# Performance work log

Measured on AMD Instinct MI355X. Metric: run time of the kernel, lower is better.

## Reference

```python
import jax, jax.numpy as jnp
import numpy as np

N = 100_000
E = 1_600_000
IN_DIM = 21
HID = 256
OUT = 256


def setup_inputs() -> dict:
    key = jax.random.key(0)
    ks = jax.random.split(key, 10)
    node_scalar = jax.random.normal(ks[0], (N, IN_DIM), dtype=jnp.float32)
    edge_index = jax.random.randint(ks[1], (2, E), 0, N, dtype=jnp.int64)
    s_in = 1.0 / np.sqrt(IN_DIM)
    s_h = 1.0 / np.sqrt(HID)
    W_in = jax.random.uniform(ks[2], (IN_DIM, HID), jnp.float32, -s_in, s_in)
    b_in = jax.random.uniform(ks[3], (HID,), jnp.float32, -s_in, s_in)
    W_self = jax.random.uniform(ks[4], (HID, HID), jnp.float32, -s_h, s_h)
    b_self = jax.random.uniform(ks[5], (HID,), jnp.float32, -s_h, s_h)
    W_nei = jax.random.uniform(ks[6], (HID, HID), jnp.float32, -s_h, s_h)
    b_nei = jax.random.uniform(ks[7], (HID,), jnp.float32, -s_h, s_h)
    W_out = jax.random.uniform(ks[8], (HID, OUT), jnp.float32, -s_h, s_h)
    b_out = jax.random.uniform(ks[9], (OUT,), jnp.float32, -s_h, s_h)
    return {
        "node_scalar": node_scalar,
        "W_in": W_in, "b_in": b_in,
        "W_self": W_self, "b_self": b_self,
        "W_nei": W_nei, "b_nei": b_nei,
        "W_out": W_out, "b_out": b_out,
        "edge_index": edge_index,
    }


def reference(node_scalar, W_in, b_in, W_self, b_self, W_nei, b_nei, W_out, b_out, edge_index):
    # x = relu(Linear(node_scalar)); dropout is identity in eval mode
    x = jax.nn.relu(node_scalar @ W_in + b_in)           # (N, H)
    n = x.shape[0]
    src, dst = edge_index[0], edge_index[1]
    msg = x[src]                                          # (E, H) gather
    agg = jax.ops.segment_sum(msg, dst, num_segments=n)   # (N, H) scatter-add
    deg = jax.ops.segment_sum(jnp.ones((dst.shape[0],), dtype=x.dtype), dst, num_segments=n)
    agg = agg / jnp.maximum(deg, 1.0)[:, None]            # degree mean (clamp_min 1)
    h = jax.nn.relu(x @ W_self + b_self + agg @ W_nei + b_nei)
    g = h.mean(axis=0)                                    # global mean pool -> (H,)
    return g @ W_out + b_out                              # (OUT,)
```

## Files before the change

kernel.cpp:

```cpp
#include <hip/hip_runtime.h>
#include <hip/hip_bf16.h>

#define HID 256
#define IND 21
#define PB 6400
#define MAXB 512

typedef short short8 __attribute__((ext_vector_type(8)));
typedef float floatx16 __attribute__((ext_vector_type(16)));
typedef float floatx2 __attribute__((ext_vector_type(2)));

__device__ inline unsigned short f2bf(float f) {
  __hip_bfloat16 h = __float2bfloat16(f);
  union { __hip_bfloat16 h; unsigned short u; } c;
  c.h = h;
  return c.u;
}

__device__ inline unsigned int pk_bf16_trunc(floatx2 p) {
  union { float f; unsigned int u; } a, b;
  a.f = p.x; b.f = p.y;
  return (b.u & 0xffff0000u) | (a.u >> 16);
}

__device__ inline void acc8p(uint2 v, floatx2* a) {
  a[0] += __builtin_amdgcn_cvt_pk_f32_fp8((int)v.x, false);
  a[1] += __builtin_amdgcn_cvt_pk_f32_fp8((int)v.x, true);
  a[2] += __builtin_amdgcn_cvt_pk_f32_fp8((int)v.y, false);
  a[3] += __builtin_amdgcn_cvt_pk_f32_fp8((int)v.y, true);
}

__device__ inline short8 mk_s8(unsigned a, unsigned b, unsigned c, unsigned d) {
  union { uint4 u; short8 s; } x; x.u = make_uint4(a, b, c, d); return x.s;
}

__device__ inline short8 dec8(uint2 v) {
  unsigned w0 = pk_bf16_trunc(__builtin_amdgcn_cvt_pk_f32_fp8((int)v.x, false));
  unsigned w1 = pk_bf16_trunc(__builtin_amdgcn_cvt_pk_f32_fp8((int)v.x, true));
  unsigned w2 = pk_bf16_trunc(__builtin_amdgcn_cvt_pk_f32_fp8((int)v.y, false));
  unsigned w3 = pk_bf16_trunc(__builtin_amdgcn_cvt_pk_f32_fp8((int)v.y, true));
  return mk_s8(w0, w1, w2, w3);
}

__device__ inline void gl16(const unsigned char* g, unsigned char* l) {
  __builtin_amdgcn_global_load_lds(
      (const __attribute__((address_space(1))) unsigned char*)g,
      (__attribute__((address_space(3))) unsigned char*)l, 16, 0, 0);
}

__global__ __launch_bounds__(256) void k_front(
    const float* __restrict__ ns, const float* __restrict__ Win,
    const float* __restrict__ bin, unsigned int* __restrict__ xq,
    uint2* __restrict__ Aqx,
    const float* __restrict__ Wself, const float* __restrict__ Wnei,
    unsigned short* __restrict__ Bf16,
    const int* __restrict__ dst, int* __restrict__ bcnt,
    int N, int E, int nb2, int G1) {
  int blk = blockIdx.x;
  int tid = threadIdx.x;
  if (blk < G1) {
    __shared__ float s[8][IND];
    __shared__ float fx[8][257];
    int nb = blk * 8;
    if (tid < 8 * IND) {
      int idx = nb * IND + tid;
      s[tid / IND][tid % IND] = (idx < N * IND) ? ns[idx] : 0.f;
    }
    float w[IND];
#pragma unroll
    for (int k = 0; k < IND; k++) w[k] = Win[k * HID + tid];
    float b = bin[tid];
    __syncthreads();
#pragma unroll
    for (int j = 0; j < 8; j++) {
      float acc = b;
#pragma unroll
      for (int k = 0; k < IND; k++) acc += s[j][k] * w[k];
      fx[j][tid] = acc > 0.f ? acc : 0.f;
    }
    __syncthreads();
#pragma unroll
    for (int t = 0; t < 2; t++) {
      int wi = tid + t * 256;
      int j = wi >> 6, cw = wi & 63;
      int node = nb + j;
      if (node < N) {
        const float* fp = &fx[j][cw * 4];
        int lo = __builtin_amdgcn_cvt_pk_fp8_f32(fp[0], fp[1], 0, false);
        int full = __builtin_amdgcn_cvt_pk_fp8_f32(fp[2], fp[3], lo, true);
        xq[(size_t)node * 64 + cw] = (unsigned int)full;
      }
    }
    {
      int j = tid >> 5, u = tid & 31;
      int node = nb + j;
      if (node < N) {
        const float* fp = &fx[j][u * 8];
        int lo0 = __builtin_amdgcn_cvt_pk_fp8_f32(fp[0], fp[1], 0, false);
        int w0  = __builtin_amdgcn_cvt_pk_fp8_f32(fp[2], fp[3], lo0, true);
        int lo1 = __builtin_amdgcn_cvt_pk_fp8_f32(fp[4], fp[5], 0, false);
        int w1  = __builtin_amdgcn_cvt_pk_fp8_f32(fp[6], fp[7], lo1, true);
        int g = node >> 5, row = node & 31, c = u >> 1, hi = u & 1;
        Aqx[(size_t)(g * 16 + c) * 64 + hi * 32 + row] =
            make_uint2((unsigned)w0, (unsigned)w1);
      }
    }
  } else if (blk < G1 + 256) {
    int n = blk - G1;
    int ct = n >> 5, l5 = n & 31;
#pragma unroll
    for (int t = 0; t < 2; t++) {
      int k = tid + t * 256;
      float v = (k < HID) ? Wself[k * HID + n] : Wnei[(k - HID) * HID + n];
      int c = k >> 4, kin = k & 15;
      int lane = (kin >> 3) * 32 + l5;
      int j = kin & 7;
      Bf16[(size_t)((c * 8 + ct) * 64 + lane) * 8 + j] = f2bf(v);
    }
  } else {
    __shared__ int lh[MAXB];
    int e0 = (blk - G1 - 256) * PB;
    for (int b = tid; b < nb2; b += 256) lh[b] = 0;
    __syncthreads();
    int c = min(PB, E - e0);
    for (int i = tid; i < c; i += 256) atomicAdd(&lh[dst[e0 + i] >> 8], 1);
    __syncthreads();
    for (int b = tid; b < nb2; b += 256)
      if (lh[b]) atomicAdd(&bcnt[b], lh[b]);
  }
}

__global__ __launch_bounds__(512) void k_bscan(
    const int* __restrict__ bcnt, int* __restrict__ bbase, int* __restrict__ bcur,
    int* __restrict__ row_start, int E, int N, int nb2) {
  __shared__ int ts[512];
  int tid = threadIdx.x;
  int v = (tid < nb2) ? bcnt[tid] : 0;
  ts[tid] = v;
  __syncthreads();
  for (int off = 1; off < 512; off <<= 1) {
    int t = (tid >= off) ? ts[tid - off] : 0;
    __syncthreads();
    ts[tid] += t;
    __syncthreads();
  }
  if (tid < nb2) { bbase[tid] = ts[tid] - v; bcur[tid] = ts[tid] - v; }
  if (tid == 0) { bbase[nb2] = E; row_start[N] = E; }
}

__global__ __launch_bounds__(256) void k_part(
    const int* __restrict__ src, const int* __restrict__ dst,
    int* __restrict__ bcur, unsigned int* __restrict__ ebuf, int E, int nb2) {
  __shared__ int lh[MAXB];
  int tid = threadIdx.x;
  int e0 = blockIdx.x * PB;
  for (int b = tid; b < nb2; b += 256) lh[b] = 0;
  __syncthreads();
  int cnt = min(PB, E - e0);
  for (int i = tid; i < cnt; i += 256) atomicAdd(&lh[dst[e0 + i] >> 8], 1);
  __syncthreads();
  for (int b = tid; b < nb2; b += 256) {
    int c = lh[b];
    lh[b] = (c > 0) ? atomicAdd(&bcur[b], c) : 0;
  }
  __syncthreads();
  for (int i = tid; i < cnt; i += 256) {
    int s = src[e0 + i];
    int d = dst[e0 + i];
    int pos = atomicAdd(&lh[d >> 8], 1);
    ebuf[pos] = ((unsigned)s << 8) | ((unsigned)d & 255u);
  }
}

__global__ __launch_bounds__(256) void k_fill2(
    const unsigned int* __restrict__ ebuf, const int* __restrict__ bbase,
    int* __restrict__ row_start, int* __restrict__ csr, int N) {
  __shared__ int lcnt[256];
  __shared__ int lcur[256];
  __shared__ int ts[256];
  int b = blockIdx.x;
  int tid = threadIdx.x;
  int start = bbase[b], end = bbase[b + 1];
  lcnt[tid] = 0;
  __syncthreads();
  for (int i = start + tid; i < end; i += 256)
    atomicAdd(&lcnt[ebuf[i] & 255u], 1);
  __syncthreads();
  int v = lcnt[tid];
  ts[tid] = v;
  __syncthreads();
  for (int off = 1; off < 256; off <<= 1) {
    int t = (tid >= off) ? ts[tid - off] : 0;
    __syncthreads();
    ts[tid] += t;
    __syncthreads();
  }
  int excl = start + ts[tid] - v;
  int node = (b << 8) + tid;
  if (node < N) row_start[node] = excl;
  lcur[tid] = excl;
  __syncthreads();
  for (int i = start + tid; i < end; i += 256) {
    unsigned int e = ebuf[i];
    int pos = atomicAdd(&lcur[e & 255u], 1);
    csr[pos] = (int)(e >> 8);
  }
}

__global__ __launch_bounds__(256) void k_agg(
    const uint2* __restrict__ xq, const int* __restrict__ csr,
    const int* __restrict__ row_start, uint2* __restrict__ aggq, int N) {
  int wid = (int)((blockIdx.x * (unsigned)blockDim.x + threadIdx.x) >> 6);
  int lane = threadIdx.x & 63;
  int half = lane >> 5;
  int l32 = lane & 31;
  if (wid >= N) return;
  int start = row_start[wid];
  int end = row_start[wid + 1];
  int c = end - start;
  floatx2 a[4], b[4], d[4], e[4];
#pragma unroll
  for (int j = 0; j < 4; j++) {
    a[j] = (floatx2){0.f, 0.f}; b[j] = (floatx2){0.f, 0.f};
    d[j] = (floatx2){0.f, 0.f}; e[j] = (floatx2){0.f, 0.f};
  }
  int i = 0;
  for (; i + 8 <= c; i += 8) {
    int s0 = csr[start + i + half];
    int s1 = csr[start + i + 2 + half];
    int s2 = csr[start + i + 4 + half];
    int s3 = csr[start + i + 6 + half];
    uint2 v0 = xq[(size_t)s0 * 32 + l32];
    uint2 v1 = xq[(size_t)s1 * 32 + l32];
    uint2 v2 = xq[(size_t)s2 * 32 + l32];
    uint2 v3 = xq[(size_t)s3 * 32 + l32];
    acc8p(v0, a); acc8p(v1, b); acc8p(v2, d); acc8p(v3, e);
  }
  for (; i + 2 <= c; i += 2) {
    int s0 = csr[start + i + half];
    uint2 v0 = xq[(size_t)s0 * 32 + l32];
    acc8p(v0, a);
  }
  if ((c & 1) && half == 0) {
    int s0 = csr[start + c - 1];
    uint2 v0 = xq[(size_t)s0 * 32 + l32];
    acc8p(v0, a);
  }
#pragma unroll
  for (int j = 0; j < 4; j++) a[j] += b[j] + d[j] + e[j];

  float f[8];
#pragma unroll
  for (int j = 0; j < 4; j++) { f[2 * j] = a[j].x; f[2 * j + 1] = a[j].y; }
#pragma unroll
  for (int j = 0; j < 8; j++) f[j] += __shfl_xor(f[j], 32);

  if (half == 0) {
    float inv = 1.0f / fmaxf((float)c, 1.0f);
#pragma unroll
    for (int j = 0; j < 8; j++) f[j] *= inv;
    int lo0 = __builtin_amdgcn_cvt_pk_fp8_f32(f[0], f[1], 0, false);
    int w0  = __builtin_amdgcn_cvt_pk_fp8_f32(f[2], f[3], lo0, true);
    int lo1 = __builtin_amdgcn_cvt_pk_fp8_f32(f[4], f[5], 0, false);
    int w1  = __builtin_amdgcn_cvt_pk_fp8_f32(f[6], f[7], lo1, true);
    int g = wid >> 5, row = wid & 31, cc = l32 >> 1, hi = l32 & 1;
    aggq[(size_t)(g * 16 + cc) * 64 + hi * 32 + row] =
        make_uint2((unsigned)w0, (unsigned)w1);
  }
}

__global__ __launch_bounds__(256, 3) void k_h(
    const unsigned char* __restrict__ Aqx, const unsigned char* __restrict__ Aqagg,
    const unsigned char* __restrict__ Bf8, const float* __restrict__ bself,
    const float* __restrict__ bnei, float* __restrict__ gsum, int N) {
  __shared__ __align__(16) unsigned char As[2][8192];
  __shared__ __align__(16) unsigned char Bs[2][16384];
  __shared__ float colsum[128];
  int tid = threadIdx.x;
  int lane = tid & 63;
  int w = tid >> 6;
  int wr = w >> 1, wc = w & 1;
  int l32 = lane & 31, half = lane >> 5;
  int bx = blockIdx.x, by = blockIdx.y;
  int rowBase = bx * 128;

  if (tid < 128) colsum[tid] = 0.f;

  floatx16 acc[2][2];
#pragma unroll
  for (int i = 0; i < 2; i++)
#pragma unroll
    for (int j = 0; j < 2; j++) acc[i][j] = (floatx16)(0.f);

  size_t a_grp = (size_t)(bx * 4 + w) * 16 * 512;
  int lb = lane * 16;

  {
    const unsigned char* asrc = Aqx + a_grp + lb;
    gl16(asrc, As[0] + w * 2048);
    gl16(asrc + 1024, As[0] + w * 2048 + 1024);
#pragma unroll
    for (int fi = 0; fi < 4; fi++) {
      int cg = w;
      int ctg = by * 4 + fi;
      gl16(Bf8 + (size_t)(cg * 8 + ctg) * 1024 + lb, Bs[0] + (w * 4 + fi) * 1024);
    }
  }

  for (int ch = 0; ch < 8; ch++) {
    int buf = ch & 1;
    __syncthreads();
    if (ch < 7) {
      int cn = ch + 1;
      const unsigned char* Aq = (cn < 4) ? Aqx : Aqagg;
      const unsigned char* asrc = Aq + a_grp + (size_t)(cn & 3) * 2048 + lb;
      unsigned char* ad = As[buf ^ 1] + w * 2048;
      gl16(asrc, ad);
      gl16(asrc + 1024, ad + 1024);
#pragma unroll
      for (int fi = 0; fi < 4; fi++) {
        int cg = cn * 4 + w;
        int ctg = by * 4 + fi;
        gl16(Bf8 + (size_t)(cg * 8 + ctg) * 1024 + lb,
             Bs[buf ^ 1] + (w * 4 + fi) * 1024);
      }
    }
#pragma unroll
    for (int cl = 0; cl < 4; cl++) {
      short8 afr[2];
#pragma unroll
      for (int rt = 0; rt < 2; rt++) {
        uint2 av = *(const uint2*)&As[buf][(wr * 2 + rt) * 2048 + cl * 512 + lane * 8];
        afr[rt] = dec8(av);
      }
#pragma unroll
      for (int ctw = 0; ctw < 2; ctw++) {
        short8 bfr = *(const short8*)&Bs[buf][(cl * 4 + wc * 2 + ctw) * 1024 + lane * 16];
#pragma unroll
        for (int rt = 0; rt < 2; rt++)
          acc[rt][ctw] = __builtin_amdgcn_mfma_f32_32x32x16_bf16(
              afr[rt], bfr, acc[rt][ctw], 0, 0, 0);
      }
    }
  }

#pragma unroll
  for (int ctw = 0; ctw < 2; ctw++) {
    int lcol = (wc * 2 + ctw) * 32 + l32;
    int gcol = by * 128 + lcol;
    float bb = bself[gcol] + bnei[gcol];
    float psum = 0.f;
#pragma unroll
    for (int rt = 0; rt < 2; rt++) {
#pragma unroll
      for (int r = 0; r < 16; r++) {
        int rw = rowBase + wr * 64 + rt * 32 + (r & 3) + 8 * (r >> 2) + 4 * half;
        float v = acc[rt][ctw][r] + bb;
        v = v > 0.f ? v : 0.f;
        if (rw < N) psum += v;
      }
    }
    atomicAdd(&colsum[lcol], psum);
  }
  __syncthreads();
  if (tid < 128) atomicAdd(&gsum[by * 128 + tid], colsum[tid]);
}

__global__ __launch_bounds__(HID) void k_out(
    const float* __restrict__ gsum, const float* __restrict__ Wout,
    const float* __restrict__ bout, float* __restrict__ out, float invN) {
  __shared__ float g[HID];
  int c = threadIdx.x;
  g[c] = gsum[c] * invN;
  __syncthreads();
  float acc = bout[c];
#pragma unroll 8
  for (int k = 0; k < HID; k++) acc += g[k] * Wout[k * HID + c];
  out[c] = acc;
}

extern "C" void kernel_launch(void* const* d_in, const int* in_sizes, int n_in,
                              void* d_out, int out_size, void* d_ws, size_t ws_size,
                              hipStream_t stream) {
  const float* ns    = (const float*)d_in[0];
  const float* Win   = (const float*)d_in[1];
  const float* bin   = (const float*)d_in[2];
  const float* Wself = (const float*)d_in[3];
  const float* bself = (const float*)d_in[4];
  const float* Wnei  = (const float*)d_in[5];
  const float* bnei  = (const float*)d_in[6];
  const float* Wout  = (const float*)d_in[7];
  const float* bout  = (const float*)d_in[8];
  const int*   eidx  = (const int*)d_in[9];

  int N = in_sizes[0] / IND;
  int E = in_sizes[9] / 2;
  const int* src = eidx;
  const int* dst = eidx + E;
  int nb2 = (N + 255) >> 8;
  int nbx = (N + 127) / 128;
  size_t NGU = (size_t)nbx * 4 * 16 * 64;

  unsigned int* xq    = (unsigned int*)d_ws;
  uint2* Aqx          = (uint2*)(xq + (size_t)N * 64);
  uint2* Aqagg        = Aqx + NGU;
  unsigned short* Bf16 = (unsigned short*)(Aqagg + NGU);
  int* csr       = (int*)(Bf16 + 256 * 512);
  unsigned int* ebuf = (unsigned int*)(csr + E);
  int* row_start = (int*)(ebuf + E);
  int* bcnt      = row_start + N + 1;
  int* bbase     = bcnt + MAXB;
  int* bcur      = bbase + MAXB + 1;
  float* gsum    = (float*)(bcur + MAXB);

  hipMemsetAsync(bcnt, 0, MAXB * sizeof(int), stream);
  hipMemsetAsync(gsum, 0, HID * sizeof(float), stream);

  int G1 = (N + 7) / 8;
  int pgrid = (E + PB - 1) / PB;
  k_front<<<G1 + 256 + pgrid, 256, 0, stream>>>(
      ns, Win, bin, xq, Aqx, Wself, Wnei, Bf16, dst, bcnt, N, E, nb2, G1);

  k_bscan<<<1, 512, 0, stream>>>(bcnt, bbase, bcur, row_start, E, N, nb2);
  k_part<<<pgrid, 256, 0, stream>>>(src, dst, bcur, ebuf, E, nb2);
  k_fill2<<<nb2, 256, 0, stream>>>(ebuf, bbase, row_start, csr, N);

  int agrid = (N + 3) / 4;
  k_agg<<<agrid, 256, 0, stream>>>((const uint2*)xq, csr, row_start, Aqagg, N);

  dim3 hgrid(nbx, 2);
  k_h<<<hgrid, 256, 0, stream>>>((const unsigned char*)Aqx,
                                 (const unsigned char*)Aqagg,
                                 (const unsigned char*)Bf16,
                                 bself, bnei, gsum, N);

  k_out<<<1, HID, 0, stream>>>(gsum, Wout, bout, (float*)d_out, 1.0f / (float)N);
}
```

Before: 329.6 us.

## Write aggregation row-major, transpose in separate kernel; replace gsum atomics with partials

k_agg now writes the fp8 aggregated rows in plain row-major order, so each node's stores are contiguous, instead of scattering them into the MFMA fragment layout. A new k_tr kernel then transposes 64-node tiles through shared memory into the fragment layout that k_h expects. Separately, k_h writes per-block column sums to a partial buffer, and k_out reduces them serially, which removes the global atomics and the gsum memset. The trade-off is an extra kernel launch and an extra round trip through memory for the aggregate, plus a serial loop of about 782 iterations per thread in k_out.

```diff
diff --git a/kernel.cpp b/kernel.cpp
--- a/kernel.cpp
+++ b/kernel.cpp
@@ -209,7 +209,7 @@
 
 __global__ __launch_bounds__(256) void k_agg(
     const uint2* __restrict__ xq, const int* __restrict__ csr,
-    const int* __restrict__ row_start, uint2* __restrict__ aggq, int N) {
+    const int* __restrict__ row_start, uint2* __restrict__ aggrm, int N) {
   int wid = (int)((blockIdx.x * (unsigned)blockDim.x + threadIdx.x) >> 6);
   int lane = threadIdx.x & 63;
   int half = lane >> 5;
@@ -263,16 +263,40 @@
     int w0  = __builtin_amdgcn_cvt_pk_fp8_f32(f[2], f[3], lo0, true);
     int lo1 = __builtin_amdgcn_cvt_pk_fp8_f32(f[4], f[5], 0, false);
     int w1  = __builtin_amdgcn_cvt_pk_fp8_f32(f[6], f[7], lo1, true);
-    int g = wid >> 5, row = wid & 31, cc = l32 >> 1, hi = l32 & 1;
-    aggq[(size_t)(g * 16 + cc) * 64 + hi * 32 + row] =
-        make_uint2((unsigned)w0, (unsigned)w1);
+    aggrm[(size_t)wid * 32 + l32] = make_uint2((unsigned)w0, (unsigned)w1);
+  }
+}
+
+__global__ __launch_bounds__(256) void k_tr(
+    const uint2* __restrict__ rm, uint2* __restrict__ fr, int N) {
+  __shared__ uint2 ld[64 * 33];
+  int b = blockIdx.x;
+  int tid = threadIdx.x;
+  int n0 = b * 64;
+#pragma unroll
+  for (int j = 0; j < 8; j++) {
+    int idx = j * 256 + tid;
+    int nl = idx >> 5, u = idx & 31;
+    int node = n0 + nl;
+    uint2 v = (node < N) ? rm[(size_t)node * 32 + u] : make_uint2(0u, 0u);
+    ld[nl * 33 + u] = v;
+  }
+  __syncthreads();
+  size_t obase = (size_t)b * 2048;
+#pragma unroll
+  for (int j = 0; j < 8; j++) {
+    int oidx = j * 256 + tid;
+    int gg = oidx >> 10, rem = oidx & 1023;
+    int c = rem >> 6, hr = rem & 63, hi = hr >> 5, row = hr & 31;
+    int nl = gg * 32 + row, u = c * 2 + hi;
+    fr[obase + oidx] = ld[nl * 33 + u];
   }
 }
 
 __global__ __launch_bounds__(256, 3) void k_h(
     const unsigned char* __restrict__ Aqx, const unsigned char* __restrict__ Aqagg,
     const unsigned char* __restrict__ Bf8, const float* __restrict__ bself,
-    const float* __restrict__ bnei, float* __restrict__ gsum, int N) {
+    const float* __restrict__ bnei, float* __restrict__ hpart, int N) {
   __shared__ __align__(16) unsigned char As[2][8192];
   __shared__ __align__(16) unsigned char Bs[2][16384];
   __shared__ float colsum[128];
@@ -301,9 +325,8 @@
     gl16(asrc + 1024, As[0] + w * 2048 + 1024);
 #pragma unroll
     for (int fi = 0; fi < 4; fi++) {
-      int cg = w;
       int ctg = by * 4 + fi;
-      gl16(Bf8 + (size_t)(cg * 8 + ctg) * 1024 + lb, Bs[0] + (w * 4 + fi) * 1024);
+      gl16(Bf8 + (size_t)(w * 8 + ctg) * 1024 + lb, Bs[0] + (w * 4 + fi) * 1024);
     }
   }
 
@@ -363,15 +386,18 @@
     atomicAdd(&colsum[lcol], psum);
   }
   __syncthreads();
-  if (tid < 128) atomicAdd(&gsum[by * 128 + tid], colsum[tid]);
+  if (tid < 128) hpart[(size_t)bx * 256 + by * 128 + tid] = colsum[tid];
 }
 
 __global__ __launch_bounds__(HID) void k_out(
-    const float* __restrict__ gsum, const float* __restrict__ Wout,
-    const float* __restrict__ bout, float* __restrict__ out, float invN) {
+    const float* __restrict__ hpart, int nbx,
+    const float* __restrict__ Wout, const float* __restrict__ bout,
+    float* __restrict__ out, float invN) {
   __shared__ float g[HID];
   int c = threadIdx.x;
-  g[c] = gsum[c] * invN;
+  float s = 0.f;
+  for (int i = 0; i < nbx; i++) s += hpart[(size_t)i * 256 + c];
+  g[c] = s * invN;
   __syncthreads();
   float acc = bout[c];
 #pragma unroll 8
@@ -401,20 +427,20 @@
   int nbx = (N + 127) / 128;
   size_t NGU = (size_t)nbx * 4 * 16 * 64;
 
-  unsigned int* xq    = (unsigned int*)d_ws;
-  uint2* Aqx          = (uint2*)(xq + (size_t)N * 64);
-  uint2* Aqagg        = Aqx + NGU;
-  unsigned short* Bf16 = (unsigned short*)(Aqagg + NGU);
+  unsigned int* xq     = (unsigned int*)d_ws;
+  uint2* Aqx           = (uint2*)(xq + (size_t)N * 64);
+  uint2* Aqagg         = Aqx + NGU;
+  uint2* aggrm         = Aqagg + NGU;
+  unsigned short* Bf16 = (unsigned short*)(aggrm + (size_t)N * 32);
   int* csr       = (int*)(Bf16 + 256 * 512);
   unsigned int* ebuf = (unsigned int*)(csr + E);
   int* row_start = (int*)(ebuf + E);
   int* bcnt      = row_start + N + 1;
   int* bbase     = bcnt + MAXB;
   int* bcur      = bbase + MAXB + 1;
-  float* gsum    = (float*)(bcur + MAXB);
+  float* hpart   = (float*)(bcur + MAXB);
 
   hipMemsetAsync(bcnt, 0, MAXB * sizeof(int), stream);
-  hipMemsetAsync(gsum, 0, HID * sizeof(float), stream);
 
   int G1 = (N + 7) / 8;
   int pgrid = (E + PB - 1) / PB;
@@ -426,13 +452,17 @@
   k_fill2<<<nb2, 256, 0, stream>>>(ebuf, bbase, row_start, csr, N);
 
   int agrid = (N + 3) / 4;
-  k_agg<<<agrid, 256, 0, stream>>>((const uint2*)xq, csr, row_start, Aqagg, N);
+  k_agg<<<agrid, 256, 0, stream>>>((const uint2*)xq, csr, row_start, aggrm, N);
+
+  int tgrid = (N + 63) / 64;
+  k_tr<<<tgrid, 256, 0, stream>>>(aggrm, Aqagg, N);
 
   dim3 hgrid(nbx, 2);
   k_h<<<hgrid, 256, 0, stream>>>((const unsigned char*)Aqx,
                                  (const unsigned char*)Aqagg,
                                  (const unsigned char*)Bf16,
-                                 bself, bnei, gsum, N);
-
-  k_out<<<1, HID, 0, stream>>>(gsum, Wout, bout, (float*)d_out, 1.0f / (float)N);
-}
+                                 bself, bnei, hpart, N);
+
+  k_out<<<1, HID, 0, stream>>>(hpart, nbx, Wout, bout, (float*)d_out,
+                               1.0f / (float)N);
+}
```

After: 482.5 us. 1.46x slower.
